# Optimization experiments

Measured on AMD Instinct MI355X. Metric: run time of the kernel, lower is better.

Reference implementation:

```python
import jax, jax.numpy as jnp
import numpy as np
import math

B, S, D, H = 2, 2048, 1024, 16
DH = D // H

def setup_inputs() -> dict:
    key = jax.random.key(0)
    k = jax.random.split(key, 6)
    scale = 1.0 / math.sqrt(D)
    x = jax.random.normal(k[0], (B, S, D), jnp.float32)
    mask = jnp.ones((B, S), jnp.int32)
    # torch.nn.Linear weights: [out_features, in_features]
    W_q = jax.random.normal(k[1], (D, D), jnp.float32) * scale
    b_q = jnp.zeros((D,), jnp.float32)
    W_v = jax.random.normal(k[2], (D, D), jnp.float32) * scale
    W_out = jax.random.normal(k[3], (D, D), jnp.float32) * scale
    b_out = jnp.zeros((D,), jnp.float32)
    return {"x": x, "W_q": W_q, "b_q": b_q, "W_v": W_v, "W_out": W_out, "b_out": b_out, "mask": mask}

def reference(x, W_q, b_q, W_v, W_out, b_out, mask):
    inv_sqrt_dh = 1.0 / math.sqrt(DH)
    # q: [B, H, S, DH]
    q = (x @ W_q.T + b_q).reshape(B, S, H, DH).transpose(0, 2, 1, 3)
    # L2-distance attention logits: -(||q_s||^2 - 2 q_s.q_t + ||q_t||^2)/sqrt(dh)
    sq = jnp.sum(q * q, axis=-1)  # [B, H, S]
    qk = jnp.einsum('bhsd,bhtd->bhst', q, q)  # [B, H, S, S]
    logits = -(sq[..., :, None] - 2.0 * qk + sq[..., None, :]) * inv_sqrt_dh
    logits = jnp.where(mask[:, None, None, :] == 0, jnp.float32(-9e15), logits)
    w = jax.nn.softmax(logits, axis=-1)  # [B, H, S, S]
    # W_q_T[h, j, i] = W_q[i, h*DH + j] -> [H, DH, D]
    W_q_T = W_q.reshape(D, H, DH).transpose(1, 2, 0)
    # v[h, i, j] = W_v[i, h*DH + j] -> [H, D, DH]
    v = W_v.reshape(D, H, DH).transpose(1, 0, 2)
    attn = jnp.einsum('bhst,bhtd->bhsd', w, q)          # [B, H, S, DH]
    attn = jnp.einsum('bhsd,hde->bhse', attn, W_q_T)    # [B, H, S, D]
    attn = jnp.einsum('bhse,hef->bhsf', attn, v) * inv_sqrt_dh  # [B, H, S, DH]
    attn = attn.transpose(0, 2, 1, 3).reshape(B, S, D)
    return x + attn @ W_out.T + b_out
```

## Files before the change

### kernel.cpp

```cpp
#include <hip/hip_runtime.h>

#define S_LEN 2048
#define D_DIM 1024
#define NH    16
#define DHEAD 64

typedef float f32x4 __attribute__((ext_vector_type(4)));
typedef __bf16 bf16x8 __attribute__((ext_vector_type(8)));
typedef unsigned short u16;
typedef unsigned int u32;
typedef unsigned short u16x8 __attribute__((ext_vector_type(8)));
typedef unsigned short u16x4 __attribute__((ext_vector_type(4)));

__device__ __forceinline__ u16 f2bf(float f) {
    union { float f; unsigned u; } c; c.f = f;
    unsigned u = c.u + 0x7fffu + ((c.u >> 16) & 1u);
    return (u16)(u >> 16);
}

#if __has_builtin(__builtin_amdgcn_exp2f)
#define EXP2(x) __builtin_amdgcn_exp2f(x)
#else
#define EXP2(x) exp2f(x)
#endif

#define C_QK  0.36067376022224085f
#define C_SQ  0.18033688011112043f

#define MFMA16(a, b, c) __builtin_amdgcn_mfma_f32_16x16x32_bf16((a), (b), (c), 0, 0, 0)

__device__ __forceinline__ u32 pack_bf(float lo, float hi) {
    union { float f; u32 u; } a, b; a.f = lo; b.f = hi;
    return (b.u & 0xFFFF0000u) | (a.u >> 16);
}

__global__ __launch_bounds__(256) void k_precomp_M(
    const float* __restrict__ Wq, const float* __restrict__ Wv, float* __restrict__ Mpart) {
    __shared__ float Qp[128][64];
    __shared__ float Vp[128][64];
    const int tid = threadIdx.x;
    const int z = blockIdx.x, h = blockIdx.y;
    {
        int r = tid >> 1, hf = tid & 1;
        const float* q = Wq + (size_t)(z * 128 + r) * D_DIM + h * DHEAD + hf * 32;
        const float* v = Wv + (size_t)(z * 128 + r) * D_DIM + h * DHEAD + hf * 32;
#pragma unroll
        for (int i = 0; i < 8; ++i) {
            *(f32x4*)&Qp[r][hf * 32 + i * 4] = *(const f32x4*)(q + i * 4);
            *(f32x4*)&Vp[r][hf * 32 + i * 4] = *(const f32x4*)(v + i * 4);
        }
    }
    __syncthreads();
    const int j0 = (tid >> 4) * 4;
    const int f0 = (tid & 15) * 4;
    f32x4 acc[4];
    const f32x4 z4 = {0.f, 0.f, 0.f, 0.f};
#pragma unroll
    for (int i = 0; i < 4; ++i) acc[i] = z4;
    for (int e = 0; e < 128; ++e) {
        f32x4 qv = *(const f32x4*)&Qp[e][j0];
        f32x4 vv = *(const f32x4*)&Vp[e][f0];
#pragma unroll
        for (int jj = 0; jj < 4; ++jj)
            acc[jj] += qv[jj] * vv;
    }
    float* dst = Mpart + (size_t)z * (NH * 64 * 64) + ((size_t)(h * 64 + j0)) * 64 + f0;
#pragma unroll
    for (int jj = 0; jj < 4; ++jj) {
        f32x4 o = acc[jj] * 0.125f;
        *(f32x4*)(dst + jj * 64) = o;
    }
}

__global__ __launch_bounds__(256) void k_precomp_W2(
    const float* __restrict__ Mpart, const float* __restrict__ Wout, u16* __restrict__ W2) {
    __shared__ float Ms[64][65];
    __shared__ float Ws[64][65];
    const int tid = threadIdx.x;
    const int ob = blockIdx.x, h = blockIdx.y;
    {
        int rr = tid >> 2, seg = tid & 3;
        const size_t mo = ((size_t)(h * 64 + rr)) * 64 + seg * 16;
        const float* ws = Wout + (size_t)(ob * 64 + rr) * D_DIM + h * DHEAD + seg * 16;
#pragma unroll
        for (int e = 0; e < 16; ++e) {
            float s = 0.f;
#pragma unroll
            for (int k = 0; k < 8; ++k) s += Mpart[mo + e + (size_t)k * 65536];
            Ms[rr][seg * 16 + e] = s;
            Ws[rr][seg * 16 + e] = ws[e];
        }
    }
    __syncthreads();
    int j = tid & 63, o0 = (tid >> 6) * 16;
    for (int oo = o0; oo < o0 + 16; ++oo) {
        float acc = 0.f;
#pragma unroll
        for (int f = 0; f < 64; ++f) acc += Ms[j][f] * Ws[oo][f];
        W2[(size_t)(ob * 64 + oo) * D_DIM + h * DHEAD + j] = f2bf(acc);
    }
}

__global__ __launch_bounds__(512, 4) void k_qproj(
    const float* __restrict__ x, const float* __restrict__ Wq,
    const float* __restrict__ bq, const int* __restrict__ mask,
    u16* __restrict__ Qbf, u16* __restrict__ QT, float* __restrict__ sq05) {
    __shared__ __align__(16) char smem[38912];
    u16* Al = (u16*)smem;
    u16* Bl = (u16*)(smem + 18432);
    float* sqp = (float*)(smem + 36864);

    const int tid = threadIdx.x, lane = tid & 63, w = tid >> 6;
    const int wm = w & 1, wn = w >> 1;
    const int col16 = lane & 15, quad = lane >> 4;
    const int bm = blockIdx.x, bn = blockIdx.y;

    f32x4 acc[4][2];
    const f32x4 z4 = {0.f, 0.f, 0.f, 0.f};
#pragma unroll
    for (int i = 0; i < 4; ++i)
#pragma unroll
        for (int j = 0; j < 2; ++j) acc[i][j] = z4;

    const int ar = tid >> 2, as = tid & 3;
    const float* pa = x + (size_t)(bm * 128 + ar) * D_DIM + as * 16;
    const float* pb = Wq + (size_t)(bn * 128 + ar) * D_DIM + as * 16;

    f32x4 fa[4], fb[4];
#pragma unroll
    for (int i = 0; i < 4; ++i) {
        fa[i] = *(const f32x4*)(pa + i * 4);
        fb[i] = *(const f32x4*)(pb + i * 4);
    }

    for (int k0 = 0; k0 < D_DIM; k0 += 64) {
        u16x8 wa[2], wb[2];
#pragma unroll
        for (int i = 0; i < 2; ++i)
#pragma unroll
            for (int e = 0; e < 4; ++e) {
                wa[i][e] = f2bf(fa[2 * i][e]); wa[i][e + 4] = f2bf(fa[2 * i + 1][e]);
                wb[i][e] = f2bf(fb[2 * i][e]); wb[i][e + 4] = f2bf(fb[2 * i + 1][e]);
            }
        __syncthreads();
#pragma unroll
        for (int i = 0; i < 2; ++i) *(u16x8*)&Al[ar * 72 + as * 16 + i * 8] = wa[i];
#pragma unroll
        for (int i = 0; i < 2; ++i) *(u16x8*)&Bl[ar * 72 + as * 16 + i * 8] = wb[i];
        __syncthreads();
        if (k0 + 64 < D_DIM) {
#pragma unroll
            for (int i = 0; i < 4; ++i) {
                fa[i] = *(const f32x4*)(pa + k0 + 64 + i * 4);
                fb[i] = *(const f32x4*)(pb + k0 + 64 + i * 4);
            }
        }
#pragma unroll
        for (int kh = 0; kh < 2; ++kh) {
            bf16x8 af[4];
#pragma unroll
            for (int mt = 0; mt < 4; ++mt)
                af[mt] = *(const bf16x8*)&Al[(wm * 64 + mt * 16 + col16) * 72 + kh * 32 + quad * 8];
#pragma unroll
            for (int nt = 0; nt < 2; ++nt) {
                bf16x8 bfr = *(const bf16x8*)&Bl[(wn * 32 + nt * 16 + col16) * 72 + kh * 32 + quad * 8];
#pragma unroll
                for (int mt = 0; mt < 4; ++mt)
                    acc[mt][nt] = MFMA16(af[mt], bfr, acc[mt][nt]);
            }
        }
    }

    const int hh = wn >> 1;
    f32x4 ssum[4];
#pragma unroll
    for (int mt = 0; mt < 4; ++mt) ssum[mt] = z4;

    u16 qv16[2][4][4];
#pragma unroll
    for (int nt = 0; nt < 2; ++nt) {
        int col = bn * 128 + wn * 32 + nt * 16 + col16;
        float bqv = bq[col];
#pragma unroll
        for (int mt = 0; mt < 4; ++mt) {
            int row0 = bm * 128 + wm * 64 + mt * 16 + quad * 4;
#pragma unroll
            for (int rr = 0; rr < 4; ++rr) {
                float qv = acc[mt][nt][rr] + bqv;
                ssum[mt][rr] += qv * qv;
                u16 bv = f2bf(qv);
                qv16[nt][mt][rr] = bv;
                Qbf[(size_t)(row0 + rr) * D_DIM + col] = bv;
            }
        }
    }
    float vred[4][4];
#pragma unroll
    for (int mt = 0; mt < 4; ++mt)
#pragma unroll
        for (int rr = 0; rr < 4; ++rr) {
            float v = ssum[mt][rr];
            v += __shfl_xor(v, 1); v += __shfl_xor(v, 2);
            v += __shfl_xor(v, 4); v += __shfl_xor(v, 8);
            vred[mt][rr] = v;
        }
    if (col16 == 0) {
#pragma unroll
        for (int mt = 0; mt < 4; ++mt)
#pragma unroll
            for (int rr = 0; rr < 4; ++rr)
                sqp[wn * 128 + wm * 64 + mt * 16 + quad * 4 + rr] = vred[mt][rr];
    }
    __syncthreads();

    u16* Td = (u16*)smem;
#pragma unroll
    for (int nt = 0; nt < 2; ++nt) {
        int dloc = (wn & 1) * 32 + nt * 16 + col16;
#pragma unroll
        for (int mt = 0; mt < 4; ++mt) {
            int sl = wm * 64 + mt * 16 + quad * 4;
#pragma unroll
            for (int rr = 0; rr < 4; ++rr)
                Td[(hh * 64 + dloc) * 130 + sl + rr] = qv16[nt][mt][rr];
        }
    }
    __syncthreads();

    const int bb = (bm * 128) >> 11, s0 = (bm * 128) & 2047;
    if (tid < 256) {
        int r = tid & 127, hh2 = tid >> 7;
        float v = sqp[(2 * hh2) * 128 + r] + sqp[(2 * hh2 + 1) * 128 + r];
        int sidx = s0 + r;
        float o = mask[bb * S_LEN + sidx] ? v * C_SQ : 1e30f;
        sq05[((size_t)(bb * NH + bn * 2 + hh2)) * S_LEN + sidx] = o;
    }
    {
        int dr = tid >> 2, ch = tid & 3;
        int hh3 = dr >> 6, d = dr & 63;
        u16* dst = QT + ((size_t)(bb * NH + bn * 2 + hh3) * DHEAD + d) * S_LEN + s0 + ch * 32;
        const u16* src = Td + (hh3 * 64 + d) * 130 + ch * 32;
#pragma unroll
        for (int i = 0; i < 4; ++i)
            *(u16x8*)(dst + i * 8) = *(const u16x8*)(src + i * 8);
    }
}

__global__ __launch_bounds__(256, 2) void k_flash(
    const u16* __restrict__ Qbf, const u16* __restrict__ QT,
    const float* __restrict__ sq05, u16* __restrict__ attnO) {
    __shared__ __align__(16) char smem[34816];
    u16* Kt  = (u16*)smem;
    u16* KtT = (u16*)(smem + 16384);
    float* sql = (float*)(smem + 32768);

    const int tid = threadIdx.x, lane = tid & 63, w = tid >> 6;
    const int col16 = lane & 15, quad = lane >> 4;
    const int wq = w & 1, wk = w >> 1;
    const int bh = blockIdx.x & 31;
    const int qt = blockIdx.x >> 5;
    const int h = bh & 15;
    const int b = bh >> 4;
    const u16* qbase = Qbf + (size_t)b * S_LEN * D_DIM + h * DHEAD;
    const u16* qtbase = QT + ((size_t)(b * NH + h)) * DHEAD * S_LEN;
    const float* sqb = sq05 + ((size_t)(b * NH + h)) * S_LEN;

    bf16x8 qb[4][2];
#pragma unroll
    for (int nq = 0; nq < 4; ++nq)
#pragma unroll
        for (int k0 = 0; k0 < 2; ++k0)
            qb[nq][k0] = *(const bf16x8*)(qbase +
                (size_t)(qt * 128 + wq * 64 + nq * 16 + col16) * D_DIM + k0 * 32 + quad * 8);

    const int r00 = wk * 64 + (col16 >> 2) * 8 + (col16 & 3);
    const int swzA = (col16 & 3) | (((col16 >> 2) & 1) << 2);
    const int krow00 = r00 * 64 + (quad ^ swzA) * 8;
    const int sq00 = wk * 64 + quad * 8;
    int vrow[4];
#pragma unroll
    for (int dblk = 0; dblk < 4; ++dblk) {
        int rT = dblk * 16 + col16;
        vrow[dblk] = rT * 128 + ((wk * 8 + quad) ^ (rT & 7)) * 8;
    }

    const int kr = tid >> 1, ks = tid & 1;
    const int td = tid >> 2, ts = tid & 3;
    const int kswz = (kr & 3) | (((kr >> 3) & 1) << 2);
    const int tswz = td & 7;
    const u16* ksrc = qbase + (size_t)kr * D_DIM + ks * 32;
    const u16* tsrc = qtbase + (size_t)td * S_LEN + ts * 32;

    u16x8 pk[4], pt[4];
    float sv = 0.f;
#pragma unroll
    for (int i = 0; i < 4; ++i) pk[i] = *(const u16x8*)(ksrc + i * 8);
#pragma unroll
    for (int i = 0; i < 4; ++i) pt[i] = *(const u16x8*)(tsrc + i * 8);
    if (tid < 128) sv = sqb[tid];

    f32x4 Oacc[4][4], lacc[4];
    const f32x4 z4 = {0.f, 0.f, 0.f, 0.f};
#pragma unroll
    for (int n = 0; n < 4; ++n) {
        lacc[n] = z4;
#pragma unroll
        for (int d = 0; d < 4; ++d) Oacc[d][n] = z4;
    }
    bf16x8 ones;
    {
        union { u16x8 u; bf16x8 b; } cv;
#pragma unroll
        for (int e = 0; e < 8; ++e) cv.u[e] = 0x3F80;
        ones = cv.b;
    }

    for (int j = 0; j < S_LEN / 128; ++j) {
        __syncthreads();
#pragma unroll
        for (int i = 0; i < 4; ++i)
            *(u16x8*)(Kt + kr * 64 + ((ks * 4 + i) ^ kswz) * 8) = pk[i];
#pragma unroll
        for (int i = 0; i < 4; ++i)
            *(u16x8*)(KtT + td * 128 + ((ts * 4 + i) ^ tswz) * 8) = pt[i];
        if (tid < 128) sql[tid] = sv;
        __syncthreads();

        int jn = (j + 1) & 15;
        {
            const u16* kn = ksrc + (size_t)jn * 128 * D_DIM;
            const u16* tn = tsrc + (size_t)jn * 128;
#pragma unroll
            for (int i = 0; i < 4; ++i) pk[i] = *(const u16x8*)(kn + i * 8);
#pragma unroll
            for (int i = 0; i < 4; ++i) pt[i] = *(const u16x8*)(tn + i * 8);
            if (tid < 128) sv = sqb[jn * 128 + tid];
        }

        for (int kt = 0; kt < 2; ++kt) {
            f32x4 sacc[2][4];
#pragma unroll
            for (int kbh = 0; kbh < 2; ++kbh)
#pragma unroll
                for (int nq = 0; nq < 4; ++nq) sacc[kbh][nq] = z4;
#pragma unroll
            for (int kbh = 0; kbh < 2; ++kbh) {
                int kro = krow00 + kt * 2048 + kbh * 256;
                bf16x8 a0 = *(const bf16x8*)(Kt + kro);
                bf16x8 a1 = *(const bf16x8*)(Kt + (kro ^ 32));
#pragma unroll
                for (int nq = 0; nq < 4; ++nq) {
                    sacc[kbh][nq] = MFMA16(a0, qb[nq][0], sacc[kbh][nq]);
                    sacc[kbh][nq] = MFMA16(a1, qb[nq][1], sacc[kbh][nq]);
                }
            }

            bf16x8 va[4];
#pragma unroll
            for (int dblk = 0; dblk < 4; ++dblk)
                va[dblk] = *(const bf16x8*)(KtT + (vrow[dblk] ^ (kt * 32)));

            u32 pf[4][4];
#pragma unroll
            for (int kbh = 0; kbh < 2; ++kbh) {
                f32x4 sqv = *(const f32x4*)(sql + sq00 + kt * 32 + kbh * 4);
#pragma unroll
                for (int nq = 0; nq < 4; ++nq) {
                    float p0 = EXP2(fmaf(sacc[kbh][nq][0], C_QK, -sqv[0]));
                    float p1 = EXP2(fmaf(sacc[kbh][nq][1], C_QK, -sqv[1]));
                    float p2 = EXP2(fmaf(sacc[kbh][nq][2], C_QK, -sqv[2]));
                    float p3 = EXP2(fmaf(sacc[kbh][nq][3], C_QK, -sqv[3]));
                    pf[nq][kbh * 2]     = pack_bf(p0, p1);
                    pf[nq][kbh * 2 + 1] = pack_bf(p2, p3);
                }
            }

#pragma unroll
            for (int nq = 0; nq < 4; ++nq) {
                union { u32 u[4]; bf16x8 b; } pb;
#pragma unroll
                for (int i = 0; i < 4; ++i) pb.u[i] = pf[nq][i];
                lacc[nq] = MFMA16(ones, pb.b, lacc[nq]);
#pragma unroll
                for (int dblk = 0; dblk < 4; ++dblk)
                    Oacc[dblk][nq] = MFMA16(va[dblk], pb.b, Oacc[dblk][nq]);
            }
        }
    }

    __syncthreads();
    float* Obuf = (float*)smem;
    float* lred = (float*)(smem + 32768);
    if (wk == 1) {
#pragma unroll
        for (int dblk = 0; dblk < 4; ++dblk)
#pragma unroll
            for (int nq = 0; nq < 4; ++nq)
                *(f32x4*)(Obuf + ((wq * 16 + dblk * 4 + nq) * 64 + lane) * 4) = Oacc[dblk][nq];
#pragma unroll
        for (int nq = 0; nq < 4; ++nq)
            lred[(wq * 4 + nq) * 64 + lane] = lacc[nq][0];
    }
    __syncthreads();
    if (wk == 0) {
        float rinv[4];
#pragma unroll
        for (int nq = 0; nq < 4; ++nq)
            rinv[nq] = 1.f / (lacc[nq][0] + lred[(wq * 4 + nq) * 64 + lane]);
        u16* obase = attnO + (size_t)b * S_LEN * D_DIM + h * DHEAD;
#pragma unroll
        for (int dblk = 0; dblk < 4; ++dblk)
#pragma unroll
            for (int nq = 0; nq < 4; ++nq) {
                f32x4 o = Oacc[dblk][nq] + *(const f32x4*)(Obuf + ((wq * 16 + dblk * 4 + nq) * 64 + lane) * 4);
                int q = qt * 128 + wq * 64 + nq * 16 + col16;
                u16x4 pkk;
#pragma unroll
                for (int rr = 0; rr < 4; ++rr) pkk[rr] = f2bf(o[rr] * rinv[nq]);
                *(u16x4*)(obase + (size_t)q * D_DIM + dblk * 16 + quad * 4) = pkk;
            }
    }
}

__global__ __launch_bounds__(512, 4) void k_oproj(
    const u16* __restrict__ attnO, const u16* __restrict__ W2,
    const float* __restrict__ x, const float* __restrict__ bout, float* __restrict__ out) {
    __shared__ __align__(16) char smem[36864];
    u16* Al = (u16*)smem;
    u16* Bl = (u16*)(smem + 18432);
    const int tid = threadIdx.x, lane = tid & 63, w = tid >> 6;
    const int wm = w & 1, wn = w >> 1;
    const int col16 = lane & 15, quad = lane >> 4;
    const int bm = blockIdx.x, bn = blockIdx.y;

    f32x4 acc[4][2];
    const f32x4 z4 = {0.f, 0.f, 0.f, 0.f};
#pragma unroll
    for (int i = 0; i < 4; ++i)
#pragma unroll
        for (int j = 0; j < 2; ++j) acc[i][j] = z4;

    const int ar = tid >> 2, as = tid & 3;
    const u16* pa = attnO + (size_t)(bm * 128 + ar) * D_DIM + as * 16;
    const u16* pb = W2 + (size_t)(bn * 128 + ar) * D_DIM + as * 16;

    u16x8 ra[2], rb[2];
#pragma unroll
    for (int i = 0; i < 2; ++i) ra[i] = *(const u16x8*)(pa + i * 8);
#pragma unroll
    for (int i = 0; i < 2; ++i) rb[i] = *(const u16x8*)(pb + i * 8);

    for (int k0 = 0; k0 < D_DIM; k0 += 64) {
        __syncthreads();
#pragma unroll
        for (int i = 0; i < 2; ++i) *(u16x8*)&Al[ar * 72 + as * 16 + i * 8] = ra[i];
#pragma unroll
        for (int i = 0; i < 2; ++i) *(u16x8*)&Bl[ar * 72 + as * 16 + i * 8] = rb[i];
        __syncthreads();
        if (k0 + 64 < D_DIM) {
#pragma unroll
            for (int i = 0; i < 2; ++i) ra[i] = *(const u16x8*)(pa + k0 + 64 + i * 8);
#pragma unroll
            for (int i = 0; i < 2; ++i) rb[i] = *(const u16x8*)(pb + k0 + 64 + i * 8);
        }
#pragma unroll
        for (int kh = 0; kh < 2; ++kh) {
            bf16x8 af[4];
#pragma unroll
            for (int mt = 0; mt < 4; ++mt)
                af[mt] = *(const bf16x8*)&Al[(wm * 64 + mt * 16 + col16) * 72 + kh * 32 + quad * 8];
#pragma unroll
            for (int nt = 0; nt < 2; ++nt) {
                bf16x8 bfr = *(const bf16x8*)&Bl[(wn * 32 + nt * 16 + col16) * 72 + kh * 32 + quad * 8];
#pragma unroll
                for (int mt = 0; mt < 4; ++mt)
                    acc[mt][nt] = MFMA16(af[mt], bfr, acc[mt][nt]);
            }
        }
    }
#pragma unroll
    for (int nt = 0; nt < 2; ++nt) {
        int col = bn * 128 + wn * 32 + nt * 16 + col16;
        float bv = bout[col];
#pragma unroll
        for (int mt = 0; mt < 4; ++mt) {
            int row0 = bm * 128 + wm * 64 + mt * 16 + quad * 4;
#pragma unroll
            for (int rr = 0; rr < 4; ++rr) {
                size_t idx = (size_t)(row0 + rr) * D_DIM + col;
                out[idx] = acc[mt][nt][rr] + x[idx] + bv;
            }
        }
    }
}

extern "C" void kernel_launch(void* const* d_in, const int* in_sizes, int n_in,
                              void* d_out, int out_size, void* d_ws, size_t ws_size,
                              hipStream_t stream) {
    const float* x    = (const float*)d_in[0];
    const float* Wq   = (const float*)d_in[1];
    const float* bq   = (const float*)d_in[2];
    const float* Wv   = (const float*)d_in[3];
    const float* Wout = (const float*)d_in[4];
    const float* bout = (const float*)d_in[5];
    const int*   mask = (const int*)d_in[6];
    float* out = (float*)d_out;

    char* ws = (char*)d_ws;
    u16*   Qbf   = (u16*)(ws);
    u16*   QT    = (u16*)(ws + (8u << 20));
    u16*   attnO = (u16*)(ws + (16u << 20));
    u16*   W2    = (u16*)(ws + (24u << 20));
    float* Mpart = (float*)(ws + (26u << 20));
    float* sq05  = (float*)(ws + (28u << 20));

    k_precomp_M<<<dim3(8, 16), dim3(256), 0, stream>>>(Wq, Wv, Mpart);
    k_precomp_W2<<<dim3(16, 16), dim3(256), 0, stream>>>(Mpart, Wout, W2);
    k_qproj<<<dim3(32, 8), dim3(512), 0, stream>>>(x, Wq, bq, mask, Qbf, QT, sq05);
    k_flash<<<dim3(512), dim3(256), 0, stream>>>(Qbf, QT, sq05, attnO);
    k_oproj<<<dim3(32, 8), dim3(512), 0, stream>>>(attnO, W2, x, bout, out);
}
```

Measured before the change: 204.3 us.

## Merge weight precompute kernels into qproj and flash launches as extra blocks

Folds the M = Wq·Wv per-head precompute into the Q-projection kernel as 128 extra blocks, and the W2 = M·Wout precompute into the flash-attention kernel as 256 extra blocks. This cuts the launch count from five to three and lets the small weight-preprocessing work run alongside the main kernels instead of serially before them. The M precompute is restructured for 512 threads, processing 64-row chunks in two passes. The trade-off is that the side blocks can compete with the main blocks for compute units and may extend the tail of each launch.

```diff
diff --git a/kernel.cpp b/kernel.cpp
--- a/kernel.cpp
+++ b/kernel.cpp
@@ -34,86 +34,55 @@
     return (b.u & 0xFFFF0000u) | (a.u >> 16);
 }
 
-__global__ __launch_bounds__(256) void k_precomp_M(
-    const float* __restrict__ Wq, const float* __restrict__ Wv, float* __restrict__ Mpart) {
-    __shared__ float Qp[128][64];
-    __shared__ float Vp[128][64];
+__global__ __launch_bounds__(512, 4) void k_mega1(
+    const float* __restrict__ x, const float* __restrict__ Wq,
+    const float* __restrict__ Wv, const float* __restrict__ bq,
+    const int* __restrict__ mask, u16* __restrict__ Qbf, u16* __restrict__ QT,
+    float* __restrict__ sq05, float* __restrict__ Mpart) {
+    __shared__ __align__(16) char smem[38912];
     const int tid = threadIdx.x;
-    const int z = blockIdx.x, h = blockIdx.y;
-    {
-        int r = tid >> 1, hf = tid & 1;
-        const float* q = Wq + (size_t)(z * 128 + r) * D_DIM + h * DHEAD + hf * 32;
-        const float* v = Wv + (size_t)(z * 128 + r) * D_DIM + h * DHEAD + hf * 32;
-#pragma unroll
-        for (int i = 0; i < 8; ++i) {
-            *(f32x4*)&Qp[r][hf * 32 + i * 4] = *(const f32x4*)(q + i * 4);
-            *(f32x4*)&Vp[r][hf * 32 + i * 4] = *(const f32x4*)(v + i * 4);
-        }
-    }
-    __syncthreads();
-    const int j0 = (tid >> 4) * 4;
-    const int f0 = (tid & 15) * 4;
-    f32x4 acc[4];
-    const f32x4 z4 = {0.f, 0.f, 0.f, 0.f};
-#pragma unroll
-    for (int i = 0; i < 4; ++i) acc[i] = z4;
-    for (int e = 0; e < 128; ++e) {
-        f32x4 qv = *(const f32x4*)&Qp[e][j0];
-        f32x4 vv = *(const f32x4*)&Vp[e][f0];
-#pragma unroll
-        for (int jj = 0; jj < 4; ++jj)
-            acc[jj] += qv[jj] * vv;
-    }
-    float* dst = Mpart + (size_t)z * (NH * 64 * 64) + ((size_t)(h * 64 + j0)) * 64 + f0;
-#pragma unroll
-    for (int jj = 0; jj < 4; ++jj) {
-        f32x4 o = acc[jj] * 0.125f;
-        *(f32x4*)(dst + jj * 64) = o;
-    }
-}
-
-__global__ __launch_bounds__(256) void k_precomp_W2(
-    const float* __restrict__ Mpart, const float* __restrict__ Wout, u16* __restrict__ W2) {
-    __shared__ float Ms[64][65];
-    __shared__ float Ws[64][65];
-    const int tid = threadIdx.x;
-    const int ob = blockIdx.x, h = blockIdx.y;
-    {
-        int rr = tid >> 2, seg = tid & 3;
-        const size_t mo = ((size_t)(h * 64 + rr)) * 64 + seg * 16;
-        const float* ws = Wout + (size_t)(ob * 64 + rr) * D_DIM + h * DHEAD + seg * 16;
-#pragma unroll
-        for (int e = 0; e < 16; ++e) {
-            float s = 0.f;
-#pragma unroll
-            for (int k = 0; k < 8; ++k) s += Mpart[mo + e + (size_t)k * 65536];
-            Ms[rr][seg * 16 + e] = s;
-            Ws[rr][seg * 16 + e] = ws[e];
-        }
-    }
-    __syncthreads();
-    int j = tid & 63, o0 = (tid >> 6) * 16;
-    for (int oo = o0; oo < o0 + 16; ++oo) {
-        float acc = 0.f;
-#pragma unroll
-        for (int f = 0; f < 64; ++f) acc += Ms[j][f] * Ws[oo][f];
-        W2[(size_t)(ob * 64 + oo) * D_DIM + h * DHEAD + j] = f2bf(acc);
-    }
-}
-
-__global__ __launch_bounds__(512, 4) void k_qproj(
-    const float* __restrict__ x, const float* __restrict__ Wq,
-    const float* __restrict__ bq, const int* __restrict__ mask,
-    u16* __restrict__ Qbf, u16* __restrict__ QT, float* __restrict__ sq05) {
-    __shared__ __align__(16) char smem[38912];
+
+    if (blockIdx.x >= 256) {
+        const int id = blockIdx.x - 256;
+        const int z = id & 7, h = id >> 3;
+        float* Qp = (float*)smem;
+        float* Vp = (float*)(smem + 16384);
+        const int r = tid >> 3, seg = tid & 7;
+        const int j0 = (tid >> 4) * 2;
+        const int f0 = (tid & 15) * 4;
+        f32x4 acc0 = {0.f, 0.f, 0.f, 0.f}, acc1 = acc0;
+        for (int c = 0; c < 2; ++c) {
+            const int e0 = z * 128 + c * 64;
+            __syncthreads();
+            const float* q = Wq + (size_t)(e0 + r) * D_DIM + h * DHEAD + seg * 8;
+            const float* v = Wv + (size_t)(e0 + r) * D_DIM + h * DHEAD + seg * 8;
+            *(f32x4*)&Qp[r * 64 + seg * 8]     = *(const f32x4*)q;
+            *(f32x4*)&Qp[r * 64 + seg * 8 + 4] = *(const f32x4*)(q + 4);
+            *(f32x4*)&Vp[r * 64 + seg * 8]     = *(const f32x4*)v;
+            *(f32x4*)&Vp[r * 64 + seg * 8 + 4] = *(const f32x4*)(v + 4);
+            __syncthreads();
+#pragma unroll 8
+            for (int e = 0; e < 64; ++e) {
+                float q0 = Qp[e * 64 + j0], q1 = Qp[e * 64 + j0 + 1];
+                f32x4 vv = *(const f32x4*)&Vp[e * 64 + f0];
+                acc0 += q0 * vv;
+                acc1 += q1 * vv;
+            }
+        }
+        float* dst = Mpart + (size_t)z * 65536 + ((size_t)(h * 64 + j0)) * 64 + f0;
+        *(f32x4*)dst        = acc0 * 0.125f;
+        *(f32x4*)(dst + 64) = acc1 * 0.125f;
+        return;
+    }
+
     u16* Al = (u16*)smem;
     u16* Bl = (u16*)(smem + 18432);
     float* sqp = (float*)(smem + 36864);
 
-    const int tid = threadIdx.x, lane = tid & 63, w = tid >> 6;
+    const int lane = tid & 63, w = tid >> 6;
     const int wm = w & 1, wn = w >> 1;
     const int col16 = lane & 15, quad = lane >> 4;
-    const int bm = blockIdx.x, bn = blockIdx.y;
+    const int bm = blockIdx.x & 31, bn = blockIdx.x >> 5;
 
     f32x4 acc[4][2];
     const f32x4 z4 = {0.f, 0.f, 0.f, 0.f};
@@ -246,15 +215,48 @@
     }
 }
 
-__global__ __launch_bounds__(256, 2) void k_flash(
+__global__ __launch_bounds__(256, 2) void k_mega2(
     const u16* __restrict__ Qbf, const u16* __restrict__ QT,
-    const float* __restrict__ sq05, u16* __restrict__ attnO) {
+    const float* __restrict__ sq05, u16* __restrict__ attnO,
+    const float* __restrict__ Mpart, const float* __restrict__ Wout,
+    u16* __restrict__ W2) {
     __shared__ __align__(16) char smem[34816];
+    const int tid = threadIdx.x;
+
+    if (blockIdx.x >= 512) {
+        const int id = blockIdx.x - 512;
+        const int ob = id & 15, h = id >> 4;
+        float* Ms = (float*)smem;
+        float* Ws = (float*)(smem + 16640);
+        {
+            int rr = tid >> 2, seg = tid & 3;
+            const size_t mo = ((size_t)(h * 64 + rr)) * 64 + seg * 16;
+            const float* ws = Wout + (size_t)(ob * 64 + rr) * D_DIM + h * DHEAD + seg * 16;
+#pragma unroll
+            for (int e = 0; e < 16; ++e) {
+                float s = 0.f;
+#pragma unroll
+                for (int k = 0; k < 8; ++k) s += Mpart[mo + e + (size_t)k * 65536];
+                Ms[rr * 65 + seg * 16 + e] = s;
+                Ws[rr * 65 + seg * 16 + e] = ws[e];
+            }
+        }
+        __syncthreads();
+        int j = tid & 63, o0 = (tid >> 6) * 16;
+        for (int oo = o0; oo < o0 + 16; ++oo) {
+            float acc = 0.f;
+#pragma unroll
+            for (int f = 0; f < 64; ++f) acc += Ms[j * 65 + f] * Ws[oo * 65 + f];
+            W2[(size_t)(ob * 64 + oo) * D_DIM + h * DHEAD + j] = f2bf(acc);
+        }
+        return;
+    }
+
     u16* Kt  = (u16*)smem;
     u16* KtT = (u16*)(smem + 16384);
     float* sql = (float*)(smem + 32768);
 
-    const int tid = threadIdx.x, lane = tid & 63, w = tid >> 6;
+    const int lane = tid & 63, w = tid >> 6;
     const int col16 = lane & 15, quad = lane >> 4;
     const int wq = w & 1, wk = w >> 1;
     const int bh = blockIdx.x & 31;
@@ -514,9 +516,7 @@
     float* Mpart = (float*)(ws + (26u << 20));
     float* sq05  = (float*)(ws + (28u << 20));
 
-    k_precomp_M<<<dim3(8, 16), dim3(256), 0, stream>>>(Wq, Wv, Mpart);
-    k_precomp_W2<<<dim3(16, 16), dim3(256), 0, stream>>>(Mpart, Wout, W2);
-    k_qproj<<<dim3(32, 8), dim3(512), 0, stream>>>(x, Wq, bq, mask, Qbf, QT, sq05);
-    k_flash<<<dim3(512), dim3(256), 0, stream>>>(Qbf, QT, sq05, attnO);
+    k_mega1<<<dim3(384), dim3(512), 0, stream>>>(x, Wq, Wv, bq, mask, Qbf, QT, sq05, Mpart);
+    k_mega2<<<dim3(768), dim3(256), 0, stream>>>(Qbf, QT, sq05, attnO, Mpart, Wout, W2);
     k_oproj<<<dim3(32, 8), dim3(512), 0, stream>>>(attnO, W2, x, bout, out);
 }
```

After: 184.6 us. 9.6% less time.
